# Kernel tuning notes

Measured on AMD Instinct MI355X. Metric: run time of the kernel, lower is better.

Reference implementation:

```python
import jax, jax.numpy as jnp
import numpy as np

B, T, C = 1, 2048, 2048
N_HEAD, N_KV = 32, 8
HD = C // N_HEAD            # 64
N_REP = N_HEAD // N_KV      # 4
WINDOW = 512                # sliding_window
N_GLOBAL = 16               # n_global_tokens


def setup_inputs() -> dict:
    key = jax.random.key(0)
    ks = jax.random.split(key, 5)
    x = jax.random.normal(ks[0], (B, T, C), jnp.float32)
    # standard RoPE frequency tables, shape (T, HD//2)
    inv_freq = 1.0 / (10000.0 ** (np.arange(0, HD, 2, dtype=np.float32) / HD))
    ang = np.outer(np.arange(T, dtype=np.float32), inv_freq)
    freqs_cos = jnp.asarray(np.cos(ang), jnp.float32)
    freqs_sin = jnp.asarray(np.sin(ang), jnp.float32)
    s = 0.02
    wq = jax.random.normal(ks[1], (C, C), jnp.float32) * s
    wk = jax.random.normal(ks[2], (N_KV * HD, C), jnp.float32) * s
    wv = jax.random.normal(ks[3], (N_KV * HD, C), jnp.float32) * s
    wo = jax.random.normal(ks[4], (C, C), jnp.float32) * s
    return {"x": x, "freqs_cos": freqs_cos, "freqs_sin": freqs_sin,
            "wq": wq, "wk": wk, "wv": wv, "wo": wo}


def _apply_rope(xh, fc, fs):
    # xh: (B, H, T, HD); fc/fs: (T, HD//2) broadcast over (B, H)
    xr = xh.reshape(*xh.shape[:-1], HD // 2, 2)
    x0, x1 = xr[..., 0], xr[..., 1]
    fc = fc[None, None]
    fs = fs[None, None]
    out = jnp.stack([x0 * fc - x1 * fs, x0 * fs + x1 * fc], axis=-1)
    return out.reshape(xh.shape)


def reference(x, freqs_cos, freqs_sin, wq, wk, wv, wo):
    Bx, Tx, Cx = x.shape
    q = (x @ wq.T).reshape(Bx, Tx, N_HEAD, HD).transpose(0, 2, 1, 3)   # (B,Hq,T,hd)
    k = (x @ wk.T).reshape(Bx, Tx, N_KV, HD).transpose(0, 2, 1, 3)     # (B,Hkv,T,hd)
    v = (x @ wv.T).reshape(Bx, Tx, N_KV, HD).transpose(0, 2, 1, 3)
    q = _apply_rope(q, freqs_cos, freqs_sin)
    k = _apply_rope(k, freqs_cos, freqs_sin)

    # GQA: group query heads over shared kv heads instead of repeat_kv
    qg = q.reshape(Bx, N_KV, N_REP, Tx, HD)
    scale = 1.0 / float(np.sqrt(HD))
    scores = jnp.einsum('bgrqd,bgkd->bgrqk', qg, k) * scale  # (B,G,R,T,T)

    # sliding-window causal mask with global tokens (kv_cache=None branch)
    q_pos = jnp.arange(Tx)[:, None]
    k_pos = jnp.arange(Tx)[None, :]
    mask = (k_pos <= q_pos) & (k_pos >= q_pos - (WINDOW - 1))
    mask = mask | (k_pos < N_GLOBAL)
    # note: global columns combined with causal rows always leave >=1 valid key
    scores = jnp.where(mask[None, None, None], scores, -jnp.inf)
    probs = jax.nn.softmax(scores, axis=-1)

    y = jnp.einsum('bgrqk,bgkd->bgrqd', probs, v)
    y = y.reshape(Bx, N_HEAD, Tx, HD).transpose(0, 2, 1, 3).reshape(Bx, Tx, Cx)
    return y @ wo.T  # dropout p=0 in eval
```

## Files before the change

kernel.cpp:

```cpp
#include <hip/hip_runtime.h>
#include <hip/hip_bf16.h>

using short4v = __attribute__((ext_vector_type(4))) short;
using short8 = __attribute__((ext_vector_type(8))) short;
using f32x4  = __attribute__((ext_vector_type(4))) float;
using f32x16 = __attribute__((ext_vector_type(16))) float;
using int4v  = __attribute__((ext_vector_type(4))) int;

#define T_SEQ  2048
#define C_DIM  2048
#define NH     32
#define NKV    8
#define HD     64
#define WINDOW 512
#define NGLOB  16

__device__ inline ushort f2bf(float f) {
  union { float f; unsigned u; } v; v.f = f;
  unsigned u = v.u;
  u += 0x7fffu + ((u >> 16) & 1u);
  return (ushort)(u >> 16);
}
__device__ inline float bf2f(ushort h) {
  union { unsigned u; float f; } v; v.u = ((unsigned)h) << 16;
  return v.f;
}
__device__ inline float max3f(float a, float b, float c) { return fmaxf(fmaxf(a, b), c); }

__device__ __forceinline__ void gl_lds16(const ushort* g, ushort* l) {
  __builtin_amdgcn_global_load_lds(
      (const __attribute__((address_space(1))) void*)g,
      (__attribute__((address_space(3))) void*)l, 16, 0, 0);
}

__device__ __forceinline__ f32x16 zero16() {
  f32x16 v;
#pragma unroll
  for (int i = 0; i < 16; i++) v[i] = 0.f;
  return v;
}

__global__ void cvt_all(const float* __restrict__ s0, ushort* __restrict__ d0, int n0,
                        const float* __restrict__ s1, ushort* __restrict__ d1, int n1,
                        const float* __restrict__ s2, ushort* __restrict__ d2, int n2,
                        const float* __restrict__ s3, ushort* __restrict__ d3, int n3,
                        const float* __restrict__ s4, ushort* __restrict__ d4, int n4) {
  int total = n0 + n1 + n2 + n3 + n4;
  int stride = gridDim.x * blockDim.x;
  for (int i = blockIdx.x * blockDim.x + threadIdx.x; i < total; i += stride) {
    int j = i; const float* s; ushort* d;
    if (j < n0) { s = s0; d = d0; }
    else { j -= n0;
      if (j < n1) { s = s1; d = d1; }
      else { j -= n1;
        if (j < n2) { s = s2; d = d2; }
        else { j -= n2;
          if (j < n3) { s = s3; d = d3; }
          else { j -= n3; s = s4; d = d4; } } } }
    f32x4 a = *reinterpret_cast<const f32x4*>(s + (size_t)j * 8);
    f32x4 b = *reinterpret_cast<const f32x4*>(s + (size_t)j * 8 + 4);
    short8 o;
#pragma unroll
    for (int k = 0; k < 4; k++) { o[k] = (short)f2bf(a[k]); o[4 + k] = (short)f2bf(b[k]); }
    *reinterpret_cast<short8*>(d + (size_t)j * 8) = o;
  }
}

template <int MODE>
__global__ __launch_bounds__(256) void gemm2p(const ushort* __restrict__ A,
                                              const ushort* __restrict__ B0,
                                              const ushort* __restrict__ B1,
                                              const ushort* __restrict__ B2,
                                              void* __restrict__ C0,
                                              void* __restrict__ C1,
                                              void* __restrict__ C2,
                                              int K) {
  __shared__ ushort As[2][2][128][32];
  __shared__ ushort Bs[2][2][64][32];
  const int tid  = threadIdx.x;
  const int lane = tid & 63;
  const int wid  = tid >> 6;
  const int wr = wid >> 1, wc = wid & 1;
  const int r16 = lane & 15, g16 = (lane >> 4) & 3;
  const int bx = blockIdx.x, by = blockIdx.y;

  const ushort* Brow;
  void* Cout;
  int ldc, col0;
  bool vtr = false;
  if constexpr (MODE == 1) {
    if (bx < 32)      { Brow = B0 + (size_t)bx * 64 * K;        Cout = C0; ldc = 2048; col0 = bx * 64; }
    else if (bx < 40) { Brow = B1 + (size_t)(bx - 32) * 64 * K; Cout = C1; ldc = 512;  col0 = (bx - 32) * 64; }
    else              { Brow = B2 + (size_t)(bx - 40) * 64 * K; Cout = C2; ldc = 512;  col0 = (bx - 40) * 64; vtr = true; }
  } else {
    Brow = B0 + (size_t)bx * 64 * K; Cout = C0; ldc = 2048; col0 = bx * 64;
  }
  const ushort* Arow = A + (size_t)by * 128 * K;

  f32x4 acc[4][2];
#pragma unroll
  for (int i = 0; i < 4; i++)
#pragma unroll
    for (int j = 0; j < 2; j++) acc[i][j] = (f32x4){0.f, 0.f, 0.f, 0.f};

  const int srow = tid >> 2, scch = tid & 3;
  const int ssc  = scch ^ ((srow >> 1) & 3);
  const int rchunk = (g16 ^ ((r16 >> 1) & 3)) * 8;

  const int nt = K >> 6;
  int d = 0;

#define STAGE(dd, k0)                                                               \
  {                                                                                 \
    gl_lds16(&Arow[(size_t)srow * K + (k0) + ssc * 8],           &As[dd][0][srow][scch * 8]);      \
    gl_lds16(&Arow[(size_t)(srow + 64) * K + (k0) + ssc * 8],    &As[dd][0][srow + 64][scch * 8]); \
    gl_lds16(&Arow[(size_t)srow * K + (k0) + 32 + ssc * 8],      &As[dd][1][srow][scch * 8]);      \
    gl_lds16(&Arow[(size_t)(srow + 64) * K + (k0) + 32 + ssc * 8], &As[dd][1][srow + 64][scch * 8]); \
    gl_lds16(&Brow[(size_t)srow * K + (k0) + ssc * 8],           &Bs[dd][0][srow][scch * 8]);      \
    gl_lds16(&Brow[(size_t)srow * K + (k0) + 32 + ssc * 8],      &Bs[dd][1][srow][scch * 8]);      \
  }

  STAGE(0, 0);
  asm volatile("s_waitcnt vmcnt(0)" ::: "memory");
  __builtin_amdgcn_s_barrier();

  for (int t = 0; t < nt; ++t) {
    if (t + 1 < nt) {
      STAGE(d ^ 1, (t + 1) * 64);
      asm volatile("s_waitcnt vmcnt(6)" ::: "memory");
    } else {
      asm volatile("s_waitcnt vmcnt(0)" ::: "memory");
    }
    __builtin_amdgcn_s_barrier();
#pragma unroll
    for (int kk = 0; kk < 2; kk++) {
      short8 af[4], bfv[2];
#pragma unroll
      for (int i = 0; i < 4; i++)
        af[i] = *reinterpret_cast<const short8*>(&As[d][kk][wr * 64 + i * 16 + r16][rchunk]);
#pragma unroll
      for (int j = 0; j < 2; j++)
        bfv[j] = *reinterpret_cast<const short8*>(&Bs[d][kk][wc * 32 + j * 16 + r16][rchunk]);
#pragma unroll
      for (int i = 0; i < 4; i++)
#pragma unroll
        for (int j = 0; j < 2; j++)
          acc[i][j] = __builtin_amdgcn_mfma_f32_16x16x32_bf16(af[i], bfv[j], acc[i][j], 0, 0, 0);
    }
    asm volatile("" ::: "memory");
    __builtin_amdgcn_s_barrier();
    d ^= 1;
  }
#undef STAGE

#pragma unroll
  for (int i = 0; i < 4; i++)
#pragma unroll
    for (int j = 0; j < 2; j++) {
      int col = col0 + wc * 32 + j * 16 + r16;
      int row0 = by * 128 + wr * 64 + i * 16 + g16 * 4;
      if (MODE == 1 && vtr) {
        short4v tv;
#pragma unroll
        for (int r = 0; r < 4; r++) tv[r] = (short)f2bf(acc[i][j][r]);
        *reinterpret_cast<short4v*>(&((ushort*)Cout)[(size_t)col * T_SEQ + row0]) = tv;
      } else {
#pragma unroll
        for (int r = 0; r < 4; r++) {
          if constexpr (MODE == 0) ((float*)Cout)[(size_t)(row0 + r) * ldc + col] = acc[i][j][r];
          else                     ((ushort*)Cout)[(size_t)(row0 + r) * ldc + col] = f2bf(acc[i][j][r]);
        }
      }
    }
}

__global__ void rope2(ushort* __restrict__ Qb, ushort* __restrict__ Kb,
                      const float* __restrict__ fc, const float* __restrict__ fs) {
  int idx = blockIdx.x * blockDim.x + threadIdx.x;
  const int QN = T_SEQ * NH * 8;
  ushort* X; int t, hh, c, ld; float ksc;
  if (idx < QN) { X = Qb; c = idx & 7; hh = (idx >> 3) & 31; t = idx >> 8; ld = NH * HD;
                  ksc = 0.125f * 1.44269504089f; }
  else { idx -= QN; X = Kb; c = idx & 7; hh = (idx >> 3) & 7; t = idx >> 6; ld = NKV * HD;
         ksc = 1.0f; }
  size_t base = (size_t)t * ld + hh * HD + c * 8;
  short8 v = *reinterpret_cast<const short8*>(&X[base]);
  f32x4 cc = *reinterpret_cast<const f32x4*>(&fc[t * 32 + c * 4]);
  f32x4 ss = *reinterpret_cast<const f32x4*>(&fs[t * 32 + c * 4]);
  short8 o;
#pragma unroll
  for (int j = 0; j < 4; j++) {
    float x0 = bf2f((ushort)v[2 * j]), x1 = bf2f((ushort)v[2 * j + 1]);
    o[2 * j]     = (short)f2bf((x0 * cc[j] - x1 * ss[j]) * ksc);
    o[2 * j + 1] = (short)f2bf((x0 * ss[j] + x1 * cc[j]) * ksc);
  }
  *reinterpret_cast<short8*>(&X[base]) = o;
}

__global__ __launch_bounds__(512) void attn32(const ushort* __restrict__ Q,
                                              const ushort* __restrict__ K,
                                              const ushort* __restrict__ Vt,
                                              ushort* __restrict__ Y) {
  __shared__ ushort Klds[2][2][2048];
  __shared__ ushort Vlds[2][2][2048];
  __shared__ float oS[4][64][33];
  __shared__ float mS[4][32];
  __shared__ float sS[4][64];
  ushort (*Ot)[32][72] = reinterpret_cast<ushort (*)[32][72]>(&oS[0][0][0]);
  const int tid  = threadIdx.x;
  const int lane = tid & 63;
  const int wv   = tid >> 6;
  const int hh   = wv & 3;
  const int split = wv >> 2;
  const int g  = blockIdx.x & 7;
  const int qt = 63 - (blockIdx.x >> 3);
  const int h  = g * 4 + hh;
  const int q0 = qt << 5;
  const int l31 = lane & 31, hi = lane >> 5;
  const int hi8 = hi << 3, hi4 = hi << 2;
  const int qrow = q0 + l31;

  short8 qf[4];
#pragma unroll
  for (int s = 0; s < 4; s++)
    qf[s] = *reinterpret_cast<const short8*>(&Q[(size_t)qrow * C_DIM + h * HD + s * 16 + hi8]);

  f32x16 o[2] = { zero16(), zero16() };
  f32x16 sacc = zero16();
  float mrow = -1e30f;
  short8 ones8;
#pragma unroll
  for (int s = 0; s < 8; s++) ones8[s] = (short)0x3F80;

  auto pack8 = [&](const float* pp) -> short8 {
    unsigned wA, wB, wC, wD;
    asm("v_cvt_pk_bf16_f32 %0, %1, %2" : "=v"(wA) : "v"(pp[0]), "v"(pp[1]));
    asm("v_cvt_pk_bf16_f32 %0, %1, %2" : "=v"(wB) : "v"(pp[2]), "v"(pp[3]));
    asm("v_cvt_pk_bf16_f32 %0, %1, %2" : "=v"(wC) : "v"(pp[4]), "v"(pp[5]));
    asm("v_cvt_pk_bf16_f32 %0, %1, %2" : "=v"(wD) : "v"(pp[6]), "v"(pp[7]));
    asm("v_permlane32_swap_b32 %0, %1" : "+v"(wA), "+v"(wC));
    asm("v_permlane32_swap_b32 %0, %1" : "+v"(wB), "+v"(wD));
    int4v w4 = { (int)wA, (int)wB, (int)wC, (int)wD };
    return __builtin_bit_cast(short8, w4);
  };

  int wsr = (q0 - (WINDOW - 1)) >> 5;
  int wstart = (wsr < 1) ? 32 : (wsr << 5);
  int ntw = (q0 >= wstart) ? (((q0 - wstart) >> 5) + 1) : 0;
  const int NT = 1 + ntw;
  const int ihalf = (NT + 1) >> 1;

#define KBOF(i) ((i) == 0 ? 0 : wstart + ((i) - 1) * 32)
#define MSK(i)  ((i) == 0 || (KBOF(i) < q0 - 480) || (KBOF(i) == q0))

  const int sp_s = tid >> 8;
  const int kr = (tid >> 3) & 31, kc = tid & 7;
  const int vr = (tid >> 2) & 63, vc = tid & 3;
  const ushort* ksrc0 = K + (size_t)kr * (NKV * HD) + g * HD + ((kc ^ (kr & 7)) * 8);
  const ushort* vsrc0 = Vt + (size_t)(g * HD + vr) * T_SEQ + ((vc ^ ((vr >> 1) & 3)) * 8);
  ushort* kdst[2] = { &Klds[sp_s][0][(tid & 255) * 8], &Klds[sp_s][1][(tid & 255) * 8] };
  ushort* vdst[2] = { &Vlds[sp_s][0][(tid & 255) * 8], &Vlds[sp_s][1][(tid & 255) * 8] };

#define STAGE(dd, i0t, i1t)                                                    \
  {                                                                            \
    int idxs = sp_s ? (i1t) : (i0t);                                           \
    if (idxs > NT - 1) idxs = NT - 1;                                          \
    int kbs = KBOF(idxs);                                                      \
    gl_lds16(ksrc0 + (size_t)kbs * (NKV * HD), kdst[dd]);                      \
    gl_lds16(vsrc0 + kbs, vdst[dd]);                                           \
  }

#define PROCESS(dd, kb, domask)                                                    \
  {                                                                                \
    short8 kf0 = *reinterpret_cast<const short8*>(                                 \
        &Klds[split][dd][l31 * 64 + (((0 * 2 + hi) ^ (l31 & 7)) * 8)]);            \
    short8 kf1 = *reinterpret_cast<const short8*>(                                 \
        &Klds[split][dd][l31 * 64 + (((1 * 2 + hi) ^ (l31 & 7)) * 8)]);            \
    short8 kf2 = *reinterpret_cast<const short8*>(                                 \
        &Klds[split][dd][l31 * 64 + (((2 * 2 + hi) ^ (l31 & 7)) * 8)]);            \
    short8 kf3 = *reinterpret_cast<const short8*>(                                 \
        &Klds[split][dd][l31 * 64 + (((3 * 2 + hi) ^ (l31 & 7)) * 8)]);            \
    f32x16 sa = zero16();                                                          \
    __builtin_amdgcn_s_setprio(1);                                                 \
    sa = __builtin_amdgcn_mfma_f32_32x32x16_bf16(kf0, qf[0], sa, 0, 0, 0);         \
    sa = __builtin_amdgcn_mfma_f32_32x32x16_bf16(kf1, qf[1], sa, 0, 0, 0);         \
    sa = __builtin_amdgcn_mfma_f32_32x32x16_bf16(kf2, qf[2], sa, 0, 0, 0);         \
    sa = __builtin_amdgcn_mfma_f32_32x32x16_bf16(kf3, qf[3], sa, 0, 0, 0);         \
    __builtin_amdgcn_s_setprio(0);                                                 \
    float p[16];                                                                   \
    _Pragma("unroll") for (int r = 0; r < 16; r++) p[r] = sa[r];                   \
    if (domask) {                                                                  \
      _Pragma("unroll") for (int r = 0; r < 16; r++) {                             \
        int kidx = (kb) + (r & 3) + 8 * (r >> 2) + hi4;                            \
        bool ok = ((kidx <= qrow) && (kidx >= qrow - (WINDOW - 1))) || (kidx < NGLOB); \
        p[r] = ok ? p[r] : -1e30f;                                                 \
      }                                                                            \
    }                                                                              \
    float m0 = max3f(p[0], p[1], p[2]);                                            \
    float m1 = max3f(p[3], p[4], p[5]);                                            \
    float m2 = max3f(p[6], p[7], p[8]);                                            \
    float m3 = max3f(p[9], p[10], p[11]);                                          \
    float m4 = max3f(p[12], p[13], p[14]);                                         \
    float tmax = fmaxf(max3f(m0, m1, m2), max3f(m3, m4, p[15]));                   \
    float pmax = fmaxf(tmax, __shfl_xor(tmax, 32));                                \
    if (!__all(pmax <= mrow + 8.0f)) {                                             \
      float mnew = fmaxf(mrow, pmax);                                              \
      float corr = exp2f(mrow - mnew);                                             \
      sacc[0] *= corr;                                                             \
      _Pragma("unroll") for (int r = 0; r < 16; r++) { o[0][r] *= corr; o[1][r] *= corr; } \
      mrow = mnew;                                                                 \
    }                                                                              \
    _Pragma("unroll") for (int r = 0; r < 16; r++) p[r] = exp2f(p[r] - mrow);      \
    short8 pb0 = pack8(&p[0]);                                                     \
    short8 pb1 = pack8(&p[8]);                                                     \
    short8 v0 = *reinterpret_cast<const short8*>(                                  \
        &Vlds[split][dd][(0 * 32 + l31) * 32 + (((0 * 2 + hi) ^ ((l31 >> 1) & 3)) * 8)]); \
    short8 v1 = *reinterpret_cast<const short8*>(                                  \
        &Vlds[split][dd][(0 * 32 + l31) * 32 + (((1 * 2 + hi) ^ ((l31 >> 1) & 3)) * 8)]); \
    short8 v2 = *reinterpret_cast<const short8*>(                                  \
        &Vlds[split][dd][(1 * 32 + l31) * 32 + (((0 * 2 + hi) ^ (((32 + l31) >> 1) & 3)) * 8)]); \
    short8 v3 = *reinterpret_cast<const short8*>(                                  \
        &Vlds[split][dd][(1 * 32 + l31) * 32 + (((1 * 2 + hi) ^ (((32 + l31) >> 1) & 3)) * 8)]); \
    __builtin_amdgcn_s_setprio(1);                                                 \
    sacc = __builtin_amdgcn_mfma_f32_32x32x16_bf16(ones8, pb0, sacc, 0, 0, 0);     \
    sacc = __builtin_amdgcn_mfma_f32_32x32x16_bf16(ones8, pb1, sacc, 0, 0, 0);     \
    o[0] = __builtin_amdgcn_mfma_f32_32x32x16_bf16(v0, pb0, o[0], 0, 0, 0);        \
    o[0] = __builtin_amdgcn_mfma_f32_32x32x16_bf16(v1, pb1, o[0], 0, 0, 0);        \
    o[1] = __builtin_amdgcn_mfma_f32_32x32x16_bf16(v2, pb0, o[1], 0, 0, 0);        \
    o[1] = __builtin_amdgcn_mfma_f32_32x32x16_bf16(v3, pb1, o[1], 0, 0, 0);        \
    __builtin_amdgcn_s_setprio(0);                                                 \
  }

  STAGE(0, 0, ihalf);
  asm volatile("s_waitcnt vmcnt(0)" ::: "memory");
  __builtin_amdgcn_s_barrier();
  int d = 0;
  for (int it = 0; it < ihalf; ++it) {
    if (it + 1 < ihalf) {
      STAGE(d ^ 1, it + 1, ihalf + it + 1);
      asm volatile("s_waitcnt vmcnt(2)" ::: "memory");
    } else {
      asm volatile("s_waitcnt vmcnt(0)" ::: "memory");
    }
    __builtin_amdgcn_s_barrier();
    int idx = split ? (ihalf + it) : it;
    if (idx < NT) {
      int kb = KBOF(idx);
      PROCESS(d, kb, MSK(idx));
    }
    asm volatile("" ::: "memory");
    __builtin_amdgcn_s_barrier();
    d ^= 1;
  }
#undef STAGE
#undef PROCESS
#undef KBOF
#undef MSK

  float ssum = sacc[0];

  if (split == 1) {
    if (hi == 0) mS[hh][l31] = mrow;
    sS[hh][lane] = ssum;
#pragma unroll
    for (int ntl = 0; ntl < 2; ntl++)
#pragma unroll
      for (int r = 0; r < 16; r++) oS[hh][lane][ntl * 16 + r] = o[ntl][r];
  }
  __syncthreads();

  float inv = 0.f;
  if (split == 0) {
    float mB = mS[hh][l31];
    float sB = sS[hh][lane];
    float mN = fmaxf(mrow, mB);
    float cA = exp2f(mrow - mN), cB = exp2f(mB - mN);
    ssum = ssum * cA + sB * cB;
#pragma unroll
    for (int ntl = 0; ntl < 2; ntl++)
#pragma unroll
      for (int r = 0; r < 16; r++)
        o[ntl][r] = o[ntl][r] * cA + oS[hh][lane][ntl * 16 + r] * cB;
    inv = 1.0f / ssum;
  }
  __syncthreads();

  if (split == 0) {
#pragma unroll
    for (int ntl = 0; ntl < 2; ntl++)
#pragma unroll
      for (int r = 0; r < 16; r++) {
        int dim = ntl * 32 + (r & 3) + 8 * (r >> 2) + hi4;
        Ot[hh][l31][dim] = f2bf(o[ntl][r] * inv);
      }
  }
  __syncthreads();

  if (split == 0) {
    int qq = lane >> 1, hf = lane & 1;
#pragma unroll
    for (int c = 0; c < 4; c++) {
      short8 vv = *reinterpret_cast<const short8*>(&Ot[hh][qq][hf * 32 + c * 8]);
      *reinterpret_cast<short8*>(&Y[(size_t)(q0 + qq) * C_DIM + h * HD + hf * 32 + c * 8]) = vv;
    }
  }
}

extern "C" void kernel_launch(void* const* d_in, const int* in_sizes, int n_in,
                              void* d_out, int out_size, void* d_ws, size_t ws_size,
                              hipStream_t stream) {
  const float* x  = (const float*)d_in[0];
  const float* fc = (const float*)d_in[1];
  const float* fs = (const float*)d_in[2];
  const float* wq = (const float*)d_in[3];
  const float* wk = (const float*)d_in[4];
  const float* wv = (const float*)d_in[5];
  const float* wo = (const float*)d_in[6];
  float* out = (float*)d_out;

  const size_t SZ_X = (size_t)T_SEQ * C_DIM;
  const size_t SZ_W = (size_t)(NKV * HD) * C_DIM;

  ushort* xb  = (ushort*)d_ws;
  ushort* wqb = xb  + SZ_X;
  ushort* wkb = wqb + SZ_X;
  ushort* wvb = wkb + SZ_W;
  ushort* wob = wvb + SZ_W;
  ushort* Qb  = wob + SZ_X;
  ushort* Kb  = Qb  + SZ_X;
  ushort* Vt  = Kb  + SZ_W;
  ushort* Yb  = Vt  + SZ_W;

  cvt_all<<<1024, 256, 0, stream>>>(x,  xb,  (int)(SZ_X / 8),
                                    wq, wqb, (int)(SZ_X / 8),
                                    wk, wkb, (int)(SZ_W / 8),
                                    wv, wvb, (int)(SZ_W / 8),
                                    wo, wob, (int)(SZ_X / 8));

  gemm2p<1><<<dim3(48, 16), 256, 0, stream>>>(xb, wqb, wkb, wvb, Qb, Kb, Vt, C_DIM);

  rope2<<<(T_SEQ * (NH + NKV) * 8) / 256, 256, 0, stream>>>(Qb, Kb, fc, fs);

  attn32<<<512, 512, 0, stream>>>(Qb, Kb, Vt, Yb);

  gemm2p<0><<<dim3(32, 16), 256, 0, stream>>>(Yb, wob, nullptr, nullptr, out, nullptr, nullptr, C_DIM);
}
```

Before: 119.6 us.

## Fuse RoPE into QKV GEMM epilogue, remap tiles, and use packed bf16 conversion

Removes the separate RoPE kernel by applying rotary embedding and the query scale inside the QKV GEMM epilogue. Lane pairs exchange values with a cross-lane shuffle, and the cos/sin tables are read from global memory per element. The GEMM block index is remapped to group tiles, likely for better L2 locality. The hand-written waitcnt and barrier pipeline is replaced with __syncthreads. The conversion kernel now uses the hardware packed bf16 conversion instruction. Trade-offs: the simpler synchronization may reduce load/compute overlap, and the epilogue gains scattered scalar table loads.

```diff
diff --git a/kernel.cpp b/kernel.cpp
--- a/kernel.cpp
+++ b/kernel.cpp
@@ -14,6 +14,7 @@
 #define HD     64
 #define WINDOW 512
 #define NGLOB  16
+#define KLOG   0.180336880f
 
 __device__ inline ushort f2bf(float f) {
   union { float f; unsigned u; } v; v.f = f;
@@ -38,6 +39,16 @@
 #pragma unroll
   for (int i = 0; i < 16; i++) v[i] = 0.f;
   return v;
+}
+
+__device__ __forceinline__ short8 cvt8(f32x4 a, f32x4 b) {
+  unsigned w0, w1, w2, w3;
+  asm("v_cvt_pk_bf16_f32 %0, %1, %2" : "=v"(w0) : "v"(a[0]), "v"(a[1]));
+  asm("v_cvt_pk_bf16_f32 %0, %1, %2" : "=v"(w1) : "v"(a[2]), "v"(a[3]));
+  asm("v_cvt_pk_bf16_f32 %0, %1, %2" : "=v"(w2) : "v"(b[0]), "v"(b[1]));
+  asm("v_cvt_pk_bf16_f32 %0, %1, %2" : "=v"(w3) : "v"(b[2]), "v"(b[3]));
+  int4v w = { (int)w0, (int)w1, (int)w2, (int)w3 };
+  return __builtin_bit_cast(short8, w);
 }
 
 __global__ void cvt_all(const float* __restrict__ s0, ushort* __restrict__ d0, int n0,
@@ -59,10 +70,7 @@
           else { j -= n3; s = s4; d = d4; } } } }
     f32x4 a = *reinterpret_cast<const f32x4*>(s + (size_t)j * 8);
     f32x4 b = *reinterpret_cast<const f32x4*>(s + (size_t)j * 8 + 4);
-    short8 o;
-#pragma unroll
-    for (int k = 0; k < 4; k++) { o[k] = (short)f2bf(a[k]); o[4 + k] = (short)f2bf(b[k]); }
-    *reinterpret_cast<short8*>(d + (size_t)j * 8) = o;
+    *reinterpret_cast<short8*>(d + (size_t)j * 8) = cvt8(a, b);
   }
 }
 
@@ -74,6 +82,8 @@
                                               void* __restrict__ C0,
                                               void* __restrict__ C1,
                                               void* __restrict__ C2,
+                                              const float* __restrict__ fc,
+                                              const float* __restrict__ fs,
                                               int K) {
   __shared__ ushort As[2][2][128][32];
   __shared__ ushort Bs[2][2][64][32];
@@ -82,7 +92,12 @@
   const int wid  = tid >> 6;
   const int wr = wid >> 1, wc = wid & 1;
   const int r16 = lane & 15, g16 = (lane >> 4) & 3;
-  const int bx = blockIdx.x, by = blockIdx.y;
+
+  int id = blockIdx.x + blockIdx.y * gridDim.x;
+  int c8 = id & 7, rr = id >> 3;
+  int bx, by;
+  if constexpr (MODE == 1) { bx = (c8 & 3) * 12 + (rr % 12); by = (c8 >> 2) * 8 + rr / 12; }
+  else                     { bx = (c8 & 3) * 8  + (rr % 8);  by = (c8 >> 2) * 8 + rr / 8; }
 
   const ushort* Brow;
   void* Cout;
@@ -112,26 +127,19 @@
 
 #define STAGE(dd, k0)                                                               \
   {                                                                                 \
-    gl_lds16(&Arow[(size_t)srow * K + (k0) + ssc * 8],           &As[dd][0][srow][scch * 8]);      \
-    gl_lds16(&Arow[(size_t)(srow + 64) * K + (k0) + ssc * 8],    &As[dd][0][srow + 64][scch * 8]); \
-    gl_lds16(&Arow[(size_t)srow * K + (k0) + 32 + ssc * 8],      &As[dd][1][srow][scch * 8]);      \
+    gl_lds16(&Arow[(size_t)srow * K + (k0) + ssc * 8],             &As[dd][0][srow][scch * 8]);      \
+    gl_lds16(&Arow[(size_t)(srow + 64) * K + (k0) + ssc * 8],      &As[dd][0][srow + 64][scch * 8]); \
+    gl_lds16(&Arow[(size_t)srow * K + (k0) + 32 + ssc * 8],        &As[dd][1][srow][scch * 8]);      \
     gl_lds16(&Arow[(size_t)(srow + 64) * K + (k0) + 32 + ssc * 8], &As[dd][1][srow + 64][scch * 8]); \
-    gl_lds16(&Brow[(size_t)srow * K + (k0) + ssc * 8],           &Bs[dd][0][srow][scch * 8]);      \
-    gl_lds16(&Brow[(size_t)srow * K + (k0) + 32 + ssc * 8],      &Bs[dd][1][srow][scch * 8]);      \
+    gl_lds16(&Brow[(size_t)srow * K + (k0) + ssc * 8],             &Bs[dd][0][srow][scch * 8]);      \
+    gl_lds16(&Brow[(size_t)srow * K + (k0) + 32 + ssc * 8],        &Bs[dd][1][srow][scch * 8]);      \
   }
 
   STAGE(0, 0);
-  asm volatile("s_waitcnt vmcnt(0)" ::: "memory");
-  __builtin_amdgcn_s_barrier();
+  __syncthreads();
 
   for (int t = 0; t < nt; ++t) {
-    if (t + 1 < nt) {
-      STAGE(d ^ 1, (t + 1) * 64);
-      asm volatile("s_waitcnt vmcnt(6)" ::: "memory");
-    } else {
-      asm volatile("s_waitcnt vmcnt(0)" ::: "memory");
-    }
-    __builtin_amdgcn_s_barrier();
+    if (t + 1 < nt) STAGE(d ^ 1, (t + 1) * 64);
 #pragma unroll
     for (int kk = 0; kk < 2; kk++) {
       short8 af[4], bfv[2];
@@ -147,11 +155,13 @@
         for (int j = 0; j < 2; j++)
           acc[i][j] = __builtin_amdgcn_mfma_f32_16x16x32_bf16(af[i], bfv[j], acc[i][j], 0, 0, 0);
     }
-    asm volatile("" ::: "memory");
-    __builtin_amdgcn_s_barrier();
+    __syncthreads();
     d ^= 1;
   }
 #undef STAGE
+
+  const bool doRope = (MODE == 1) && !vtr;
+  const float ksc = (MODE == 1 && bx < 32) ? KLOG : 1.0f;
 
 #pragma unroll
   for (int i = 0; i < 4; i++)
@@ -164,6 +174,18 @@
 #pragma unroll
         for (int r = 0; r < 4; r++) tv[r] = (short)f2bf(acc[i][j][r]);
         *reinterpret_cast<short4v*>(&((ushort*)Cout)[(size_t)col * T_SEQ + row0]) = tv;
+      } else if (doRope) {
+        int pr = (col & 63) >> 1;
+        bool ev = ((col & 1) == 0);
+#pragma unroll
+        for (int r = 0; r < 4; r++) {
+          float a = acc[i][j][r];
+          float b = __shfl_xor(a, 1);
+          int t = row0 + r;
+          float cv = fc[t * 32 + pr], sv = fs[t * 32 + pr];
+          float v = ev ? (a * cv - b * sv) : (b * sv + a * cv);
+          ((ushort*)Cout)[(size_t)t * ldc + col] = f2bf(v * ksc);
+        }
       } else {
 #pragma unroll
         for (int r = 0; r < 4; r++) {
@@ -172,29 +194,6 @@
         }
       }
     }
-}
-
-__global__ void rope2(ushort* __restrict__ Qb, ushort* __restrict__ Kb,
-                      const float* __restrict__ fc, const float* __restrict__ fs) {
-  int idx = blockIdx.x * blockDim.x + threadIdx.x;
-  const int QN = T_SEQ * NH * 8;
-  ushort* X; int t, hh, c, ld; float ksc;
-  if (idx < QN) { X = Qb; c = idx & 7; hh = (idx >> 3) & 31; t = idx >> 8; ld = NH * HD;
-                  ksc = 0.125f * 1.44269504089f; }
-  else { idx -= QN; X = Kb; c = idx & 7; hh = (idx >> 3) & 7; t = idx >> 6; ld = NKV * HD;
-         ksc = 1.0f; }
-  size_t base = (size_t)t * ld + hh * HD + c * 8;
-  short8 v = *reinterpret_cast<const short8*>(&X[base]);
-  f32x4 cc = *reinterpret_cast<const f32x4*>(&fc[t * 32 + c * 4]);
-  f32x4 ss = *reinterpret_cast<const f32x4*>(&fs[t * 32 + c * 4]);
-  short8 o;
-#pragma unroll
-  for (int j = 0; j < 4; j++) {
-    float x0 = bf2f((ushort)v[2 * j]), x1 = bf2f((ushort)v[2 * j + 1]);
-    o[2 * j]     = (short)f2bf((x0 * cc[j] - x1 * ss[j]) * ksc);
-    o[2 * j + 1] = (short)f2bf((x0 * ss[j] + x1 * cc[j]) * ksc);
-  }
-  *reinterpret_cast<short8*>(&X[base]) = o;
 }
 
 __global__ __launch_bounds__(512) void attn32(const ushort* __restrict__ Q,
@@ -437,11 +436,10 @@
                                     wv, wvb, (int)(SZ_W / 8),
                                     wo, wob, (int)(SZ_X / 8));
 
-  gemm2p<1><<<dim3(48, 16), 256, 0, stream>>>(xb, wqb, wkb, wvb, Qb, Kb, Vt, C_DIM);
-
-  rope2<<<(T_SEQ * (NH + NKV) * 8) / 256, 256, 0, stream>>>(Qb, Kb, fc, fs);
+  gemm2p<1><<<dim3(48, 16), 256, 0, stream>>>(xb, wqb, wkb, wvb, Qb, Kb, Vt, fc, fs, C_DIM);
 
   attn32<<<512, 512, 0, stream>>>(Qb, Kb, Vt, Yb);
 
-  gemm2p<0><<<dim3(32, 16), 256, 0, stream>>>(Yb, wob, nullptr, nullptr, out, nullptr, nullptr, C_DIM);
-}
+  gemm2p<0><<<dim3(32, 16), 256, 0, stream>>>(Yb, wob, nullptr, nullptr, out, nullptr, nullptr,
+                                              fc, fs, C_DIM);
+}
```

Measured after the change: 116.2 us, median of 3. 2.8% less time.
